# Performance work log

Measured on AMD Instinct MI355X. Metric: run time of the kernel, lower is better.

## Reference

```python
import jax, jax.numpy as jnp
import numpy as np

BS, LATENT, HID, MAXLEN = 128, 512, 1024, 512

def setup_inputs() -> dict:
    key = jax.random.key(0)
    ks = jax.random.split(key, 12)
    s = 1.0 / np.sqrt(HID)  # pytorch default LSTM init scale
    inp = {}
    inp["decoder_input"] = jax.random.normal(ks[0], (BS, LATENT), jnp.float32)
    inp["lengths"] = jax.random.randint(ks[1], (BS,), 0, MAXLEN)
    # bidirectional single-layer LSTM params (gate order i,f,g,o; combined bias = b_ih+b_hh)
    inp["Wih_f"] = jax.random.uniform(ks[2], (4 * HID, LATENT), jnp.float32, -s, s)
    inp["Whh_f"] = jax.random.uniform(ks[3], (4 * HID, HID), jnp.float32, -s, s)
    inp["b_f"] = jax.random.uniform(ks[4], (4 * HID,), jnp.float32, -s, s)
    inp["Wih_b"] = jax.random.uniform(ks[5], (4 * HID, LATENT), jnp.float32, -s, s)
    inp["Whh_b"] = jax.random.uniform(ks[6], (4 * HID, HID), jnp.float32, -s, s)
    inp["b_b"] = jax.random.uniform(ks[7], (4 * HID,), jnp.float32, -s, s)
    # out: Linear(hidden -> latent); fc1: Linear(2*hidden -> 1)
    inp["W_out"] = jax.random.uniform(ks[8], (LATENT, HID), jnp.float32, -s, s)
    inp["b_out"] = jax.random.uniform(ks[9], (LATENT,), jnp.float32, -s, s)
    inp["W_fc1"] = jax.random.uniform(ks[10], (1, 2 * HID), jnp.float32, -s, s)
    inp["b_fc1"] = jax.random.uniform(ks[11], (1,), jnp.float32, -s, s)
    return inp

def _lstm_cell(x, h, c, Wih, Whh, b):
    z = x @ Wih.T + h @ Whh.T + b  # (bs, 4H)
    i, f, g, o = jnp.split(z, 4, axis=-1)
    c2 = jax.nn.sigmoid(f) * c + jax.nn.sigmoid(i) * jnp.tanh(g)
    h2 = jax.nn.sigmoid(o) * jnp.tanh(c2)
    return h2, c2

def reference(decoder_input, lengths, Wih_f, Whh_f, b_f, Wih_b, Whh_b, b_b,
              W_out, b_out, W_fc1, b_fc1):
    max_len = int(jnp.max(lengths))  # static decode length
    bs = decoder_input.shape[0]
    h0 = jnp.zeros((bs, HID), decoder_input.dtype)

    def step(carry, _):
        x, hf, cf, hb, cb = carry
        # bidirectional LSTM over a length-1 sequence = two cells on same input
        hf, cf = _lstm_cell(x, hf, cf, Wih_f, Whh_f, b_f)
        hb, cb = _lstm_cell(x, hb, cb, Wih_b, Whh_b, b_b)
        out_t = jnp.concatenate([hf, hb], axis=-1)  # (bs, 2H)
        # next input = out(h_n[-1]) i.e. backward-direction hidden
        x_next = hb @ W_out.T + b_out
        return (x_next, hf, cf, hb, cb), out_t

    carry0 = (decoder_input, h0, h0, h0, h0)
    _, outs = jax.lax.scan(step, carry0, xs=None, length=max_len)  # (T, bs, 2H)
    x = jnp.transpose(outs, (1, 0, 2))  # (bs, T, 2H)
    x = jax.nn.relu(x)
    return x @ W_fc1.T + b_fc1  # (bs, T, 1)
```

## Files before the change

### kernel.cpp

```cpp
#include <hip/hip_runtime.h>
#include <math.h>

typedef unsigned short u16;
typedef __attribute__((ext_vector_type(8))) short short8;
typedef __attribute__((ext_vector_type(4))) float f32x4;

__device__ __forceinline__ float sigm(float x) { return 1.0f / (1.0f + expf(-x)); }

__device__ __forceinline__ u16 f2bf(float x) {
    union { float f; unsigned u; } v; v.f = x;
    unsigned r = v.u + 0x7fffu + ((v.u >> 16) & 1u);
    return (u16)(r >> 16);
}
__device__ __forceinline__ float bf2f(u16 h) {
    union { unsigned u; float f; } v; v.u = ((unsigned)h) << 16;
    return v.f;
}
__device__ __forceinline__ f32x4 mfma16(short8 a, short8 b, f32x4 c) {
    return __builtin_amdgcn_mfma_f32_16x16x32_bf16(a, b, c, 0, 0, 0);
}
__device__ __forceinline__ void gl_lds16(const void* g, void* l) {
    __builtin_amdgcn_global_load_lds(
        (const __attribute__((address_space(1))) unsigned int*)g,
        (__attribute__((address_space(3))) unsigned int*)l, 16, 0, 0);
}
__device__ __forceinline__ int swz(int c) { return (c ^ (c >> 2)) & 3; }

#define FENCE() asm volatile("" ::: "memory")

#define STAGE_W(kk, buf)                                                      \
    gl_lds16(Wsrc + sA + (kk), sm + (buf) * 8192 + lds0)

#define LOAD_A(kk, AH_, AL_)                                                  \
    do {                                                                      \
        _Pragma("unroll") for (int ks_ = 0; ks_ < 2; ++ks_) {                 \
            AH_[ks_] = *(const short8*)(Ah + aoff + (kk) + ks_ * 32);         \
            AL_[ks_] = *(const short8*)(Al + aoff + (kk) + ks_ * 32);         \
        }                                                                     \
    } while (0)

#define COMPUTE(bix, AH_, AL_, cix)                                           \
    do {                                                                      \
        const char* bb_ = sm + (bix) * 8192;                                  \
        _Pragma("unroll") for (int ks_ = 0; ks_ < 2; ++ks_) {                 \
            short8 bh_[2], bl_[2];                                            \
            _Pragma("unroll") for (int nt_ = 0; nt_ < 2; ++nt_) {             \
                const int col_ = nt_ * 16 + l15;                              \
                const int off_ = ks_ * 2048 + col_ * 64 + ((quad ^ swz(col_)) * 16); \
                bh_[nt_] = *(const short8*)(bb_ + off_);                      \
                bl_[nt_] = *(const short8*)(bb_ + 4096 + off_);               \
            }                                                                 \
            _Pragma("unroll") for (int nt_ = 0; nt_ < 2; ++nt_) {             \
                acc[nt_] = mfma16(AH_[ks_], bh_[nt_], acc[nt_]);              \
                acc[nt_] = mfma16(AL_[ks_], bh_[nt_], acc[nt_]);              \
                acc[nt_] = mfma16(AH_[ks_], bl_[nt_], acc[nt_]);              \
            }                                                                 \
        }                                                                     \
        if (fc1w) {                                                           \
            const int kb_ = (cix) * 64 + quad * 8;                            \
            _Pragma("unroll") for (int ks_ = 0; ks_ < 2; ++ks_) {             \
                const float* wp_ = smWf + kb_ + ks_ * 32;                     \
                const f32x4 w0_ = *(const f32x4*)(wp_);                       \
                const f32x4 w1_ = *(const f32x4*)(wp_ + 4);                   \
                const short8 hv_ = AH_[ks_];                                  \
                const short8 lv_ = AL_[ks_];                                  \
                _Pragma("unroll") for (int e_ = 0; e_ < 8; ++e_) {            \
                    const float v_ = bf2f((u16)hv_[e_]) + bf2f((u16)lv_[e_]); \
                    const float wv_ = (e_ < 4) ? w0_[e_] : w1_[e_ - 4];       \
                    fsum = fmaf(fmaxf(v_, 0.0f), wv_, fsum);                  \
                }                                                             \
            }                                                                 \
        }                                                                     \
    } while (0)

#define ITER(cc, BC, BS, AHU, ALU, AHL, ALL)                                  \
    do {                                                                      \
        asm volatile("s_waitcnt vmcnt(14)" ::: "memory");                     \
        __builtin_amdgcn_s_barrier();                                         \
        FENCE();                                                              \
        STAGE_W(((cc) + 3) * 64, BS);                                         \
        FENCE();                                                              \
        LOAD_A(((cc) + 3) * 64, AHL, ALL);                                    \
        COMPUTE(BC, AHU, ALU, (cc));                                          \
    } while (0)

__global__ __launch_bounds__(512, 2) void k_step(
    const u16* __restrict__ Ah, const u16* __restrict__ Al,
    u16* __restrict__ NAh, u16* __restrict__ NAl,
    const u16* __restrict__ WH, const u16* __restrict__ WL, int wstride,
    int koff_f, int nch_f, int koff_b, int nch_b,
    const float* __restrict__ BR, float* __restrict__ CF, float* __restrict__ CB,
    const float* __restrict__ Wfc1, const float* __restrict__ bfc1,
    float* __restrict__ out, int T, int t)
{
    __shared__ __align__(16) char sm[32768];
    __shared__ __align__(16) char ze[18432];
    __shared__ __align__(16) float smWf[2048];

    const int tid = threadIdx.x, bid = blockIdx.x;
    const int w = tid >> 6, lane = tid & 63, l15 = lane & 15, quad = lane >> 4;
    const int dir = bid & 1;
    const int colgrp = bid >> 1;
    const int nbase = dir * 4096 + colgrp * 32;
    const int koff = dir ? koff_b : koff_f;
    const int nch  = dir ? nch_b : nch_f;
    const int r0 = w * 16;

    const bool fc1b = (dir == 0) && (colgrp == 0);
    const bool fc1w = fc1b && (t > 0);

    const int sp = w >> 2, skh = (w >> 1) & 1, ci = w & 1;
    const u16* Wsrc = sp ? WL : WH;
    size_t sA;
    int lds0;
    {
        const int col = ci * 16 + (lane >> 2);
        const int s = (lane & 3) ^ swz(col);
        sA = (size_t)(nbase + col) * wstride + (size_t)(koff + skh * 32 + s * 8);
        lds0 = sp * 4096 + skh * 2048 + ci * 1024;
    }

    const size_t aoff = (size_t)(r0 + l15) * 2048 + (size_t)(koff + quad * 8);

    f32x4 acc[2] = {};
    short8 ah0[2], al0[2], ah1[2], al1[2];
    short8 ah2[2], al2[2], ah3[2], al3[2];
    float fsum = 0.0f;

    if (fc1b && tid < 256) {
        const f32x4 w0 = *(const f32x4*)(Wfc1 + tid * 8);
        const f32x4 w1 = *(const f32x4*)(Wfc1 + tid * 8 + 4);
        *(f32x4*)(smWf + tid * 8) = w0;
        *(f32x4*)(smWf + tid * 8 + 4) = w1;
    }
    asm volatile("s_waitcnt vmcnt(0) lgkmcnt(0)" ::: "memory");

    STAGE_W(0, 0);   FENCE(); LOAD_A(0, ah0, al0);   FENCE();
    STAGE_W(64, 1);  FENCE(); LOAD_A(64, ah1, al1);  FENCE();
    STAGE_W(128, 2); FENCE(); LOAD_A(128, ah2, al2); FENCE();

    for (int c = 0; c < nch; c += 4) {
        ITER(c + 0, 0, 3, ah0, al0, ah3, al3);
        ITER(c + 1, 1, 0, ah1, al1, ah0, al0);
        ITER(c + 2, 2, 1, ah2, al2, ah1, al1);
        ITER(c + 3, 3, 2, ah3, al3, ah2, al2);
    }
    asm volatile("s_waitcnt vmcnt(0)" ::: "memory");

    if (fc1w) {
        float v = fsum;
        v += __shfl_xor(v, 16);
        v += __shfl_xor(v, 32);
        if (lane < 16)
            out[(size_t)(r0 + l15) * T + (t - 1)] = v + bfc1[0];
    }

    char* zb = ze + w * 2304;
#pragma unroll
    for (int nt = 0; nt < 2; ++nt)
#pragma unroll
        for (int r = 0; r < 4; ++r)
            *(float*)(zb + (quad * 4 + r) * 144 + (nt * 16 + l15) * 4) = acc[nt][r];

    float* C = dir ? CB : CF;
    const int ul = lane & 7;
#pragma unroll
    for (int p2 = 0; p2 < 2; ++p2) {
        const int ml = p2 * 8 + (lane >> 3);
        const f32x4 z = *(const f32x4*)(zb + ml * 144 + ul * 16);
        const f32x4 b4 = *(const f32x4*)(BR + nbase + ul * 4);
        const float zi = z[0] + b4[0], zf = z[1] + b4[1];
        const float zg = z[2] + b4[2], zo = z[3] + b4[3];
        const int u = colgrp * 8 + ul;
        const int m = r0 + ml;
        const size_t cidx = (size_t)m * 1024 + u;
        const float cold = C[cidx];
        const float c2 = sigm(zf) * cold + sigm(zi) * tanhf(zg);
        const float h2 = sigm(zo) * tanhf(c2);
        C[cidx] = c2;
        const size_t hidx = (size_t)m * 2048 + dir * 1024 + u;
        const u16 hh = f2bf(h2);
        NAh[hidx] = hh;
        NAl[hidx] = f2bf(h2 - bf2f(hh));
    }
}

__global__ __launch_bounds__(256) void k_tail(
    const u16* __restrict__ Ah, const u16* __restrict__ Al,
    const float* __restrict__ Wfc1, const float* __restrict__ bfc1,
    float* __restrict__ out, int T)
{
    __shared__ float red[256];
    const int m = blockIdx.x, tid = threadIdx.x;
    const size_t base = (size_t)m * 2048 + tid * 8;
    const short8 hv = *(const short8*)(Ah + base);
    const short8 lv = *(const short8*)(Al + base);
    float s = 0.0f;
#pragma unroll
    for (int e = 0; e < 8; ++e) {
        const float v = bf2f((u16)hv[e]) + bf2f((u16)lv[e]);
        s = fmaf(fmaxf(v, 0.0f), Wfc1[tid * 8 + e], s);
    }
    red[tid] = s;
    __syncthreads();
    for (int off = 128; off > 0; off >>= 1) {
        if (tid < off) red[tid] += red[tid + off];
        __syncthreads();
    }
    if (tid == 0) out[(size_t)m * T + T - 1] = red[0] + bfc1[0];
}

__global__ __launch_bounds__(256, 1) void k_fold(
    const u16* __restrict__ AH, const u16* __restrict__ AL,
    const u16* __restrict__ BH, const u16* __restrict__ BL,
    const float* __restrict__ Whh_b,
    u16* __restrict__ WH, u16* __restrict__ WL)
{
    const int tid = threadIdx.x, bid = blockIdx.x;
    const int w = tid >> 6, lane = tid & 63, l15 = lane & 15, quad = lane >> 4;
    const int bm = bid >> 4, bn = bid & 15;
    const int ar0 = bm * 64 + (w & 1) * 32;
    const int br0 = bn * 64 + (w >> 1) * 32;
    f32x4 acc[2][2] = {};
    for (int k0 = 0; k0 < 512; k0 += 32) {
        short8 a_h[2], a_l[2], b_h[2], b_l[2];
#pragma unroll
        for (int mt = 0; mt < 2; ++mt) {
            const size_t o = (size_t)(ar0 + mt * 16 + l15) * 512 + k0 + quad * 8;
            a_h[mt] = *(const short8*)(AH + o);
            a_l[mt] = *(const short8*)(AL + o);
        }
#pragma unroll
        for (int nt = 0; nt < 2; ++nt) {
            const size_t o = (size_t)(br0 + nt * 16 + l15) * 512 + k0 + quad * 8;
            b_h[nt] = *(const short8*)(BH + o);
            b_l[nt] = *(const short8*)(BL + o);
        }
#pragma unroll
        for (int mt = 0; mt < 2; ++mt)
#pragma unroll
            for (int nt = 0; nt < 2; ++nt) {
                acc[mt][nt] = mfma16(a_h[mt], b_h[nt], acc[mt][nt]);
                acc[mt][nt] = mfma16(a_l[mt], b_h[nt], acc[mt][nt]);
                acc[mt][nt] = mfma16(a_h[mt], b_l[nt], acc[mt][nt]);
            }
    }
#pragma unroll
    for (int mt = 0; mt < 2; ++mt)
#pragma unroll
        for (int nt = 0; nt < 2; ++nt)
#pragma unroll
            for (int r = 0; r < 4; ++r) {
                const int row = ar0 + mt * 16 + quad * 4 + r;
                const int j = br0 + nt * 16 + l15;
                float v = acc[mt][nt][r];
                if (row >= 4096)
                    v += Whh_b[(size_t)((row & 3) * 1024 + ((row & 4095) >> 2)) * 1024 + j];
                const size_t d = (size_t)row * 2048 + 1024 + j;
                const u16 hh = f2bf(v);
                WH[d] = hh;
                WL[d] = f2bf(v - bf2f(hh));
            }
}

__global__ __launch_bounds__(256) void k_prep(
    const float* __restrict__ dec,
    const float* __restrict__ Wih_f, const float* __restrict__ Whh_f,
    const float* __restrict__ b_f, const float* __restrict__ Wih_b,
    const float* __restrict__ b_b, const float* __restrict__ W_out,
    const float* __restrict__ b_out, const float* __restrict__ b_fc1,
    u16* __restrict__ WihH, u16* __restrict__ WihL,
    u16* __restrict__ WoTH, u16* __restrict__ WoTL,
    float* __restrict__ BR0, float* __restrict__ BR1,
    u16* __restrict__ A0h, u16* __restrict__ A0l,
    u16* __restrict__ WH, u16* __restrict__ WL,
    float* __restrict__ out, int out_size)
{
    const int t = blockIdx.x * 256 + threadIdx.x;
    if (t < 524288) {
        const int colp = t >> 6, kb = (t & 63) * 8;
        const int dir = colp >> 12, u = (colp & 4095) >> 2, g = colp & 3;
        const float* src = (dir ? Wih_b : Wih_f) + (size_t)(g * 1024 + u) * 512 + kb;
        const size_t d = (size_t)colp * 512 + kb;
#pragma unroll
        for (int j = 0; j < 8; ++j) {
            const float v = src[j];
            const u16 hh = f2bf(v);
            WihH[d + j] = hh; WihL[d + j] = f2bf(v - bf2f(hh));
        }
    } else if (t < 589824) {
        const int i = t - 524288, jc = i >> 6, lb = (i & 63) * 8;
#pragma unroll
        for (int jj = 0; jj < 8; ++jj) {
            const float v = W_out[(size_t)(lb + jj) * 1024 + jc];
            const size_t d = (size_t)jc * 512 + lb + jj;
            const u16 hh = f2bf(v);
            WoTH[d] = hh; WoTL[d] = f2bf(v - bf2f(hh));
        }
    } else if (t < 598016) {
        const int colp = t - 589824;
        const int dir = colp >> 12, u = (colp & 4095) >> 2, g = colp & 3;
        const float* Wih = dir ? Wih_b : Wih_f;
        const float s = (dir ? b_b : b_f)[g * 1024 + u];
        BR0[colp] = s;
        float dot = 0.0f;
        for (int l = 0; l < 512; ++l)
            dot += Wih[(size_t)(g * 1024 + u) * 512 + l] * b_out[l];
        BR1[colp] = s + dot;
    } else if (t < 606208) {
        const int i = t - 598016, m = i >> 6, kb = (i & 63) * 8;
#pragma unroll
        for (int j = 0; j < 8; ++j) {
            const float v = dec[(size_t)m * 512 + kb + j];
            const size_t d = (size_t)m * 2048 + kb + j;
            const u16 hh = f2bf(v);
            A0h[d] = hh; A0l[d] = f2bf(v - bf2f(hh));
        }
    } else if (t < 614400) {
        const int base = (t - 606208) * 8;
        const float b0 = b_fc1[0];
#pragma unroll
        for (int j = 0; j < 8; ++j)
            if (base + j < out_size) out[base + j] = b0;
    } else {
        const int i = t - 614400, colp = i >> 7, kb = (i & 127) * 8;
        const int u = colp >> 2, g = colp & 3;
        const float* src = Whh_f + (size_t)(g * 1024 + u) * 1024 + kb;
        const size_t d = (size_t)colp * 2048 + kb;
#pragma unroll
        for (int j = 0; j < 8; ++j) {
            const float v = src[j];
            const u16 hh = f2bf(v);
            WH[d + j] = hh; WL[d + j] = f2bf(v - bf2f(hh));
        }
    }
}

extern "C" void kernel_launch(void* const* d_in, const int* in_sizes, int n_in,
                              void* d_out, int out_size, void* d_ws, size_t ws_size,
                              hipStream_t stream) {
    const float* dec   = (const float*)d_in[0];
    const float* Wih_f = (const float*)d_in[2];
    const float* Whh_f = (const float*)d_in[3];
    const float* b_f   = (const float*)d_in[4];
    const float* Wih_b = (const float*)d_in[5];
    const float* Whh_b = (const float*)d_in[6];
    const float* b_b   = (const float*)d_in[7];
    const float* W_out = (const float*)d_in[8];
    const float* b_out = (const float*)d_in[9];
    const float* W_fc1 = (const float*)d_in[10];
    const float* b_fc1 = (const float*)d_in[11];
    float* out = (float*)d_out;

    char* ws = (char*)d_ws;
    u16* WH    = (u16*)(ws);
    u16* WL    = (u16*)(ws + 33554432);
    u16* WihH  = (u16*)(ws + 67108864);
    u16* WihL  = (u16*)(ws + 75497472);
    u16* WoTH  = (u16*)(ws + 83886080);
    u16* WoTL  = (u16*)(ws + 84934656);
    u16* A0h   = (u16*)(ws + 85983232);
    u16* A0l   = (u16*)(ws + 86507520);
    u16* A1h   = (u16*)(ws + 87031808);
    u16* A1l   = (u16*)(ws + 87556096);
    float* CF  = (float*)(ws + 88080384);
    float* CB  = (float*)(ws + 88604672);
    float* BR0 = (float*)(ws + 89128960);
    float* BR1 = (float*)(ws + 89161728);

    k_prep<<<4448, 256, 0, stream>>>(dec, Wih_f, Whh_f, b_f, Wih_b, b_b,
                                     W_out, b_out, b_fc1,
                                     WihH, WihL, WoTH, WoTL, BR0, BR1,
                                     A0h, A0l, WH, WL, out, out_size);
    k_fold<<<2048, 256, 0, stream>>>(WihH, WihL, WoTH, WoTL, Whh_b, WH, WL);
    hipMemsetAsync(CF, 0, 1048576, stream);

    const int T = out_size / 128;
    u16* Abh[2] = {A0h, A1h};
    u16* Abl[2] = {A0l, A1l};
    for (int t = 0; t < T; ++t) {
        const int in = t & 1, nx = in ^ 1;
        if (t == 0) {
            k_step<<<256, 512, 0, stream>>>(A0h, A0l, A1h, A1l,
                                            WihH, WihL, 512, 0, 8, 0, 8,
                                            BR0, CF, CB, W_fc1, b_fc1, out, T, 0);
        } else {
            k_step<<<256, 512, 0, stream>>>(Abh[in], Abl[in], Abh[nx], Abl[nx],
                                            WH, WL, 2048, 0, 32, 1024, 16,
                                            BR1, CF, CB, W_fc1, b_fc1, out, T, t);
        }
    }
    k_tail<<<128, 256, 0, stream>>>(Abh[T & 1], Abl[T & 1], W_fc1, b_fc1, out, T);
}
```

Baseline: 21.64 ms.

## Retile step kernel into 1024 smaller blocks splitting rows and columns

Each recurrent step block previously handled 32 gate columns for all 128 batch rows with 8 waves. Now the batch is split in two halves and each block handles 16 columns for 64 rows with 4 waves, giving 1024 blocks of 256 threads. LDS staging, the epilogue layout and the fc1 partial-sum ownership are resized to match. The aim is more blocks in flight per CU and better latency hiding. The cost is that every weight tile is fetched twice, once per row half, which adds L2/HBM traffic per step.

```diff
diff --git a/kernel.cpp b/kernel.cpp
--- a/kernel.cpp
+++ b/kernel.cpp
@@ -29,7 +29,7 @@
 #define FENCE() asm volatile("" ::: "memory")
 
 #define STAGE_W(kk, buf)                                                      \
-    gl_lds16(Wsrc + sA + (kk), sm + (buf) * 8192 + lds0)
+    gl_lds16(Wsrc + sA + (kk), sm + (buf) * 4096 + lds0)
 
 #define LOAD_A(kk, AH_, AL_)                                                  \
     do {                                                                      \
@@ -41,20 +41,14 @@
 
 #define COMPUTE(bix, AH_, AL_, cix)                                           \
     do {                                                                      \
-        const char* bb_ = sm + (bix) * 8192;                                  \
+        const char* bb_ = sm + (bix) * 4096;                                  \
         _Pragma("unroll") for (int ks_ = 0; ks_ < 2; ++ks_) {                 \
-            short8 bh_[2], bl_[2];                                            \
-            _Pragma("unroll") for (int nt_ = 0; nt_ < 2; ++nt_) {             \
-                const int col_ = nt_ * 16 + l15;                              \
-                const int off_ = ks_ * 2048 + col_ * 64 + ((quad ^ swz(col_)) * 16); \
-                bh_[nt_] = *(const short8*)(bb_ + off_);                      \
-                bl_[nt_] = *(const short8*)(bb_ + 4096 + off_);               \
-            }                                                                 \
-            _Pragma("unroll") for (int nt_ = 0; nt_ < 2; ++nt_) {             \
-                acc[nt_] = mfma16(AH_[ks_], bh_[nt_], acc[nt_]);              \
-                acc[nt_] = mfma16(AL_[ks_], bh_[nt_], acc[nt_]);              \
-                acc[nt_] = mfma16(AH_[ks_], bl_[nt_], acc[nt_]);              \
-            }                                                                 \
+            const int off_ = ks_ * 1024 + l15 * 64 + ((quad ^ swz(l15)) * 16);\
+            const short8 bh_ = *(const short8*)(bb_ + off_);                  \
+            const short8 bl_ = *(const short8*)(bb_ + 2048 + off_);           \
+            acc = mfma16(AH_[ks_], bh_, acc);                                 \
+            acc = mfma16(AL_[ks_], bh_, acc);                                 \
+            acc = mfma16(AH_[ks_], bl_, acc);                                 \
         }                                                                     \
         if (fc1w) {                                                           \
             const int kb_ = (cix) * 64 + quad * 8;                            \
@@ -75,7 +69,7 @@
 
 #define ITER(cc, BC, BS, AHU, ALU, AHL, ALL)                                  \
     do {                                                                      \
-        asm volatile("s_waitcnt vmcnt(14)" ::: "memory");                     \
+        asm volatile("s_waitcnt vmcnt(10)" ::: "memory");                     \
         __builtin_amdgcn_s_barrier();                                         \
         FENCE();                                                              \
         STAGE_W(((cc) + 3) * 64, BS);                                         \
@@ -84,7 +78,7 @@
         COMPUTE(BC, AHU, ALU, (cc));                                          \
     } while (0)
 
-__global__ __launch_bounds__(512, 2) void k_step(
+__global__ __launch_bounds__(256, 4) void k_step(
     const u16* __restrict__ Ah, const u16* __restrict__ Al,
     u16* __restrict__ NAh, u16* __restrict__ NAl,
     const u16* __restrict__ WH, const u16* __restrict__ WL, int wstride,
@@ -93,41 +87,42 @@
     const float* __restrict__ Wfc1, const float* __restrict__ bfc1,
     float* __restrict__ out, int T, int t)
 {
-    __shared__ __align__(16) char sm[32768];
-    __shared__ __align__(16) char ze[18432];
+    __shared__ __align__(16) char sm[16384];
+    __shared__ __align__(16) char ze[4608];
     __shared__ __align__(16) float smWf[2048];
 
     const int tid = threadIdx.x, bid = blockIdx.x;
     const int w = tid >> 6, lane = tid & 63, l15 = lane & 15, quad = lane >> 4;
     const int dir = bid & 1;
-    const int colgrp = bid >> 1;
-    const int nbase = dir * 4096 + colgrp * 32;
+    const int rest = bid >> 1;
+    const int rowhalf = rest >> 8, colgrp = rest & 255;
+    const int nbase = dir * 4096 + colgrp * 16;
     const int koff = dir ? koff_b : koff_f;
     const int nch  = dir ? nch_b : nch_f;
-    const int r0 = w * 16;
+    const int r0 = rowhalf * 64 + w * 16;
 
     const bool fc1b = (dir == 0) && (colgrp == 0);
     const bool fc1w = fc1b && (t > 0);
 
-    const int sp = w >> 2, skh = (w >> 1) & 1, ci = w & 1;
+    const int sp = w >> 1, skh = w & 1;
     const u16* Wsrc = sp ? WL : WH;
     size_t sA;
     int lds0;
     {
-        const int col = ci * 16 + (lane >> 2);
+        const int col = lane >> 2;
         const int s = (lane & 3) ^ swz(col);
         sA = (size_t)(nbase + col) * wstride + (size_t)(koff + skh * 32 + s * 8);
-        lds0 = sp * 4096 + skh * 2048 + ci * 1024;
+        lds0 = sp * 2048 + skh * 1024;
     }
 
     const size_t aoff = (size_t)(r0 + l15) * 2048 + (size_t)(koff + quad * 8);
 
-    f32x4 acc[2] = {};
+    f32x4 acc = {};
     short8 ah0[2], al0[2], ah1[2], al1[2];
     short8 ah2[2], al2[2], ah3[2], al3[2];
     float fsum = 0.0f;
 
-    if (fc1b && tid < 256) {
+    if (fc1b) {
         const f32x4 w0 = *(const f32x4*)(Wfc1 + tid * 8);
         const f32x4 w1 = *(const f32x4*)(Wfc1 + tid * 8 + 4);
         *(f32x4*)(smWf + tid * 8) = w0;
@@ -155,23 +150,20 @@
             out[(size_t)(r0 + l15) * T + (t - 1)] = v + bfc1[0];
     }
 
-    char* zb = ze + w * 2304;
-#pragma unroll
-    for (int nt = 0; nt < 2; ++nt)
-#pragma unroll
-        for (int r = 0; r < 4; ++r)
-            *(float*)(zb + (quad * 4 + r) * 144 + (nt * 16 + l15) * 4) = acc[nt][r];
+    char* zb = ze + w * 1152;
+#pragma unroll
+    for (int r = 0; r < 4; ++r)
+        *(float*)(zb + (quad * 4 + r) * 72 + l15 * 4) = acc[r];
 
     float* C = dir ? CB : CF;
-    const int ul = lane & 7;
-#pragma unroll
-    for (int p2 = 0; p2 < 2; ++p2) {
-        const int ml = p2 * 8 + (lane >> 3);
-        const f32x4 z = *(const f32x4*)(zb + ml * 144 + ul * 16);
+    {
+        const int ml = lane >> 2;
+        const int ul = lane & 3;
+        const f32x4 z = *(const f32x4*)(zb + ml * 72 + ul * 16);
         const f32x4 b4 = *(const f32x4*)(BR + nbase + ul * 4);
         const float zi = z[0] + b4[0], zf = z[1] + b4[1];
         const float zg = z[2] + b4[2], zo = z[3] + b4[3];
-        const int u = colgrp * 8 + ul;
+        const int u = colgrp * 4 + ul;
         const int m = r0 + ml;
         const size_t cidx = (size_t)m * 1024 + u;
         const float cold = C[cidx];
@@ -381,13 +373,13 @@
     for (int t = 0; t < T; ++t) {
         const int in = t & 1, nx = in ^ 1;
         if (t == 0) {
-            k_step<<<256, 512, 0, stream>>>(A0h, A0l, A1h, A1l,
-                                            WihH, WihL, 512, 0, 8, 0, 8,
-                                            BR0, CF, CB, W_fc1, b_fc1, out, T, 0);
+            k_step<<<1024, 256, 0, stream>>>(A0h, A0l, A1h, A1l,
+                                             WihH, WihL, 512, 0, 8, 0, 8,
+                                             BR0, CF, CB, W_fc1, b_fc1, out, T, 0);
         } else {
-            k_step<<<256, 512, 0, stream>>>(Abh[in], Abl[in], Abh[nx], Abl[nx],
-                                            WH, WL, 2048, 0, 32, 1024, 16,
-                                            BR1, CF, CB, W_fc1, b_fc1, out, T, t);
+            k_step<<<1024, 256, 0, stream>>>(Abh[in], Abl[in], Abh[nx], Abl[nx],
+                                             WH, WL, 2048, 0, 32, 1024, 16,
+                                             BR1, CF, CB, W_fc1, b_fc1, out, T, t);
         }
     }
     k_tail<<<128, 256, 0, stream>>>(Abh[T & 1], Abl[T & 1], W_fc1, b_fc1, out, T);
```

After: 35.35 ms. 63.3% more time.
